# Kernel tuning notes

Measured on AMD Instinct MI355X. Metric: run time of the kernel, lower is better.

## Reference

```python
import jax, jax.numpy as jnp
import numpy as np

HEADS = 16
PHI = (1.0 + np.sqrt(5.0)) / 2.0


def setup_inputs() -> dict:
    key = jax.random.key(0)
    k1, k2, k3, k4 = jax.random.split(key, 4)
    B, L, D = 2, 2048, 1024
    x = jax.random.normal(k1, (B, L, D), dtype=jnp.float32)
    # nn.Linear(dim, 3*dim, bias=False): store as [D, 3D] for x @ W
    w_qkv = jax.random.normal(k2, (D, 3 * D), dtype=jnp.float32) * (D ** -0.5)
    w_proj = jax.random.normal(k3, (D, D), dtype=jnp.float32) * (D ** -0.5)
    b_proj = jax.random.normal(k4, (D,), dtype=jnp.float32) * 0.01
    return {"x": x, "w_qkv": w_qkv, "w_proj": w_proj, "b_proj": b_proj}


def phi_bias(L):
    # pos[i] = (i * phi) mod 1 ; bias = log(exp(-|pos_i - pos_j|) + 1e-8)
    pos = (jnp.arange(L, dtype=jnp.float32) * PHI) % 1.0
    dist = jnp.abs(pos[:, None] - pos[None, :])  # [L, L]
    return jnp.log(jnp.exp(-dist) + 1e-8)


def reference(x, w_qkv, w_proj, b_proj):
    B, L, D = x.shape
    H = HEADS
    Dh = D // H
    scale = Dh ** -0.5
    qkv = (x @ w_qkv).reshape(B, L, 3, H, Dh)
    q = jnp.transpose(qkv[:, :, 0], (0, 2, 1, 3))  # [B, H, L, Dh]
    k = jnp.transpose(qkv[:, :, 1], (0, 2, 1, 3))
    v = jnp.transpose(qkv[:, :, 2], (0, 2, 1, 3))
    attn = jnp.einsum("bhid,bhjd->bhij", q, k) * scale  # [B, H, L, L]
    attn = attn + phi_bias(L)[None, None]  # additive phi-distance bias
    attn = jax.nn.softmax(attn, axis=-1)
    out = jnp.einsum("bhij,bhjd->bhid", attn, v)  # [B, H, L, Dh]
    out = jnp.transpose(out, (0, 2, 1, 3)).reshape(B, L, D)
    return out @ w_proj + b_proj
```

## Files before the change

### kernel.cpp

```cpp
#include <hip/hip_runtime.h>
#include <math.h>


typedef _Float16 f16;
typedef _Float16 f16x4 __attribute__((ext_vector_type(4)));
typedef _Float16 f16x8 __attribute__((ext_vector_type(8)));
typedef float f32x4 __attribute__((ext_vector_type(4)));

#define MFMA32(a, b, c) __builtin_amdgcn_mfma_f32_16x16x32_f16(a, b, c, 0, 0, 0)

static constexpr int Bsz = 2, Lseq = 2048, Dm = 1024, H = 16, Dh = 64;
static constexpr int Mtot = Bsz * Lseq;
static constexpr int NQKV = 3 * Dm;
static constexpr float PHI_F = 1.61803398874989484820f;
static constexpr float LOG2E = 1.44269504088896f;
static constexpr float QS = 0.125f * LOG2E;
static constexpr float CSTEP = 0.55417527999932633f;

__device__ __forceinline__ void pk2(float a, float b, f16* d) {
  auto v = __builtin_amdgcn_cvt_pkrtz(a, b);
  d[0] = (f16)v[0];
  d[1] = (f16)v[1];
}

__device__ __forceinline__ void load16_to_lds(const f16* g, f16* l) {
  __builtin_amdgcn_global_load_lds(
      (const __attribute__((address_space(1))) unsigned int*)g,
      (__attribute__((address_space(3))) unsigned int*)l, 16, 0, 0);
}

__global__ __launch_bounds__(256) void prep_kernel(
    const float* __restrict__ x, const float* __restrict__ wqkv,
    const float* __restrict__ wproj, f16* __restrict__ xb,
    f16* __restrict__ wqkvT, f16* __restrict__ wpT) {
  __shared__ float tile[32][33];
  int bid = blockIdx.x, tid = threadIdx.x;
  if (bid < 4096) {
    int i = bid * 1024 + tid * 4;
    float4 v = *reinterpret_cast<const float4*>(x + i);
    f16 t[4] = {(f16)v.x, (f16)v.y, (f16)v.z, (f16)v.w};
    *reinterpret_cast<uint2*>(xb + i) = *reinterpret_cast<uint2*>(t);
    return;
  }
  const float* in;
  f16* out;
  int K, N, n0, k0;
  if (bid < 4096 + 3072) {
    int b2 = bid - 4096;
    in = wqkv; out = wqkvT; K = Dm; N = NQKV;
    n0 = (b2 % 96) * 32; k0 = (b2 / 96) * 32;
  } else {
    int b2 = bid - 7168;
    in = wproj; out = wpT; K = Dm; N = Dm;
    n0 = (b2 & 31) * 32; k0 = (b2 >> 5) * 32;
  }
  int tx = tid & 31, ty = tid >> 5;
#pragma unroll
  for (int r = 0; r < 32; r += 8)
    tile[ty + r][tx] = in[(size_t)(k0 + ty + r) * N + n0 + tx];
  __syncthreads();
#pragma unroll
  for (int r = 0; r < 32; r += 8)
    out[(size_t)(n0 + ty + r) * K + k0 + tx] = (f16)tile[tx][ty + r];
}

template <int MODE>
__global__ __launch_bounds__(256) void gemm_f16(
    const f16* __restrict__ A, const f16* __restrict__ Bt,
    int M, int N, int K,
    f16* __restrict__ qb, f16* __restrict__ kb, f16* __restrict__ vb,
    float* __restrict__ out, const float* __restrict__ bias) {
  constexpr int BM = (MODE == 0) ? 128 : 64;
  constexpr int MI = BM / 32;
  constexpr int AI = BM / 32;
  __shared__ f16 As[BM * 64];
  __shared__ f16 Bs[128 * 64];

  int tid = threadIdx.x;
  int wave = tid >> 6, lane = tid & 63;
  int quad = lane >> 4, l16 = lane & 15;
  int wm = (wave >> 1) * (MI * 16), wn = (wave & 1) * 64;

  int lid = blockIdx.x;
  int xcd = lid & 7, t = lid >> 3;
  int m0, n0;
  if (MODE == 0) {
    int mg = xcd >> 1, ng = xcd & 1;
    m0 = (mg * 8 + t / 12) * 128;
    n0 = (ng * 12 + t % 12) * 128;
  } else {
    m0 = (xcd * 8 + (t >> 3)) * 64;
    n0 = (t & 7) * 128;
  }

  const int gu = (lane & 7) ^ (lane >> 3);
  const f16* gA[AI];
  f16* lA[AI];
#pragma unroll
  for (int i = 0; i < AI; i++) {
    int it = wave * AI + i;
    gA[i] = A + (size_t)(m0 + it * 8 + (lane >> 3)) * K + gu * 8;
    lA[i] = As + it * 512;
  }
  const f16* gB[4];
  f16* lB[4];
#pragma unroll
  for (int i = 0; i < 4; i++) {
    int it = wave * 4 + i;
    gB[i] = Bt + (size_t)(n0 + it * 8 + (lane >> 3)) * K + gu * 8;
    lB[i] = Bs + it * 512;
  }

  f32x4 acc[MI][4] = {};

  for (int k0 = 0; k0 < K; k0 += 64) {
#pragma unroll
    for (int i = 0; i < AI; i++) load16_to_lds(gA[i] + k0, lA[i]);
#pragma unroll
    for (int i = 0; i < 4; i++) load16_to_lds(gB[i] + k0, lB[i]);
    __syncthreads();
#pragma unroll
    for (int s = 0; s < 2; s++) {
      f16x8 a[MI], b[4];
#pragma unroll
      for (int i = 0; i < MI; i++) {
        int row = wm + i * 16 + l16;
        a[i] = *reinterpret_cast<const f16x8*>(
            As + row * 64 + (((s * 4 + quad) ^ (l16 & 7)) * 8));
      }
#pragma unroll
      for (int j = 0; j < 4; j++) {
        int row = wn + j * 16 + l16;
        b[j] = *reinterpret_cast<const f16x8*>(
            Bs + row * 64 + (((s * 4 + quad) ^ (l16 & 7)) * 8));
      }
#pragma unroll
      for (int i = 0; i < MI; i++)
#pragma unroll
        for (int j = 0; j < 4; j++)
          acc[i][j] = MFMA32(a[i], b[j], acc[i][j]);
    }
    __syncthreads();
  }

  if (MODE == 1) {
#pragma unroll
    for (int i = 0; i < MI; i++)
#pragma unroll
      for (int j = 0; j < 4; j++) {
        int n = n0 + wn + j * 16 + l16;
#pragma unroll
        for (int r = 0; r < 4; r++) {
          int m = m0 + wm + i * 16 + quad * 4 + r;
          out[(size_t)m * N + n] = acc[i][j][r] + bias[n];
        }
      }
    return;
  }
  int ty = n0 >> 10;
  if (ty < 2) {
    f16* dst = (ty == 0) ? qb : kb;
    float sc = (ty == 0) ? QS : 1.0f;
#pragma unroll
    for (int i = 0; i < MI; i++)
#pragma unroll
      for (int j = 0; j < 4; j++) {
        int n = n0 + wn + j * 16 + l16;
        int h = (n & 1023) >> 6, dh = n & 63;
#pragma unroll
        for (int r = 0; r < 4; r++) {
          int m = m0 + wm + i * 16 + quad * 4 + r;
          int b = m >> 11, l = m & 2047;
          dst[(((size_t)(b * H + h)) * Lseq + l) * Dh + dh] =
              (f16)(acc[i][j][r] * sc);
        }
      }
  } else {
#pragma unroll
    for (int i = 0; i < MI; i++) {
      int mb = m0 + wm + i * 16 + quad * 4;
      int b = mb >> 11, l = mb & 2047;
      int L0 = l & ~63, lg = l & 63;
      int c = ((lg >> 5) << 2) | ((lg >> 2) & 3);
      int e0 = ((lg >> 4) & 1) * 4;
      int off = L0 + c * 8 + e0;
#pragma unroll
      for (int j = 0; j < 4; j++) {
        int n = n0 + wn + j * 16 + l16;
        int h = (n & 1023) >> 6, dh = n & 63;
        f16x4 v;
        pk2(acc[i][j][0], acc[i][j][1], (f16*)&v);
        pk2(acc[i][j][2], acc[i][j][3], ((f16*)&v) + 2);
        *reinterpret_cast<uint2*>(
            vb + ((size_t)(b * H + h) * Dh + dh) * Lseq + off) =
            *reinterpret_cast<uint2*>(&v);
      }
    }
  }
}

__global__ __launch_bounds__(256, 4) void attn_kernel(
    const f16* __restrict__ qb,
    const f16* __restrict__ kb,
    const f16* __restrict__ vb,
    f16* __restrict__ ctx) {
  __shared__ __align__(16) unsigned char smem[32768];
  f16* Ks0 = (f16*)smem;
  f16* Ks1 = (f16*)(smem + 8192);
  f16* Vs0 = (f16*)(smem + 16384);
  f16* Vs1 = (f16*)(smem + 24576);

  int bh = blockIdx.y;
  int q0 = blockIdx.x * 64;
  int tid = threadIdx.x, wave = tid >> 6, lane = tid & 63;
  int quad = lane >> 4, l16 = lane & 15;
  int jhalf = wave >> 1, qhalf = wave & 1;

  f16x8 qfrag[2][2];
  float pq[2];
#pragma unroll
  for (int set = 0; set < 2; set++) {
    int q = q0 + qhalf * 32 + set * 16 + l16;
    const f16* Qrow = qb + ((size_t)bh * Lseq + q) * Dh;
    qfrag[set][0] = *reinterpret_cast<const f16x8*>(Qrow + quad * 8);
    qfrag[set][1] = *reinterpret_cast<const f16x8*>(Qrow + 32 + quad * 8);
    pq[set] = fmodf((float)q * PHI_F, 1.0f);
  }

  float pk[2][4];
#pragma unroll
  for (int jb = 0; jb < 2; jb++)
#pragma unroll
    for (int r = 0; r < 4; r++) {
      int j = jhalf * 32 + jb * 16 + quad * 4 + r;
      pk[jb][r] = fmodf((float)j * PHI_F, 1.0f);
    }

  const f16* Kbh = kb + (size_t)bh * Lseq * Dh;
  const f16* Vbh = vb + (size_t)bh * Dh * Lseq;
  const int gu = (lane & 7) ^ (lane >> 3);
  const f16* gK[2];
  const f16* gV[2];
  f16* lK[2];
  f16* lV[2];
#pragma unroll
  for (int i = 0; i < 2; i++) {
    int g8 = (wave * 2 + i) * 8 + (lane >> 3);
    gK[i] = Kbh + (size_t)g8 * Dh + gu * 8;
    gV[i] = Vbh + (size_t)g8 * Lseq + gu * 8;
    lK[i] = Ks0 + (wave * 2 + i) * 512;
    lV[i] = Vs0 + (wave * 2 + i) * 512;
  }

  const f16 one = (f16)1.0f;
  const f16x8 ones8 = {one, one, one, one, one, one, one, one};

  f32x4 acc_o[2][4] = {};
  f32x4 acc_l[2] = {};

  auto phase = [&](const f16* Ksp, const f16* Vsp) {
    f32x4 accs[2][2] = {};
#pragma unroll
    for (int s = 0; s < 2; s++)
#pragma unroll
      for (int jb = 0; jb < 2; jb++) {
        f16x8 kf = *reinterpret_cast<const f16x8*>(
            Ksp + (jhalf * 32 + jb * 16 + l16) * 64 +
            (((s * 4 + quad) ^ (l16 & 7)) * 8));
        accs[0][jb] = MFMA32(kf, qfrag[0][s], accs[0][jb]);
        accs[1][jb] = MFMA32(kf, qfrag[1][s], accs[1][jb]);
      }
    f16x8 pf8[2];
#pragma unroll
    for (int set = 0; set < 2; set++) {
#pragma unroll
      for (int jb = 0; jb < 2; jb++) {
        float p[4];
#pragma unroll
        for (int r = 0; r < 4; r++) {
          float d = pq[set] - pk[jb][r];
          float arg = fmaf(-LOG2E, fabsf(d), accs[set][jb][r]);
          p[r] = __builtin_amdgcn_exp2f(arg);
        }
        pk2(p[0], p[1], ((f16*)&pf8[set]) + jb * 4);
        pk2(p[2], p[3], ((f16*)&pf8[set]) + jb * 4 + 2);
      }
      acc_l[set] = MFMA32(ones8, pf8[set], acc_l[set]);
    }
#pragma unroll
    for (int jb = 0; jb < 2; jb++)
#pragma unroll
      for (int r = 0; r < 4; r++)
        pk[jb][r] = __builtin_amdgcn_fractf(pk[jb][r] + CSTEP);
#pragma unroll
    for (int dblk = 0; dblk < 4; dblk++) {
      int row = dblk * 16 + l16;
      f16x8 va = *reinterpret_cast<const f16x8*>(
          Vsp + row * 64 + (((jhalf * 4 + quad) ^ (l16 & 7)) * 8));
      acc_o[0][dblk] = MFMA32(va, pf8[0], acc_o[0][dblk]);
      acc_o[1][dblk] = MFMA32(va, pf8[1], acc_o[1][dblk]);
    }
  };

  for (int j0 = 0; j0 < Lseq; j0 += 128) {
    __syncthreads();
#pragma unroll
    for (int i = 0; i < 2; i++) {
      load16_to_lds(gK[i] + (size_t)j0 * Dh, lK[i]);
      load16_to_lds(gK[i] + (size_t)(j0 + 64) * Dh, lK[i] + 4096);
      load16_to_lds(gV[i] + j0, lV[i]);
      load16_to_lds(gV[i] + j0 + 64, lV[i] + 4096);
    }
    __syncthreads();
    phase(Ks0, Vs0);
    phase(Ks1, Vs1);
  }

  __syncthreads();
  float* Oex = (float*)smem;
  float* Lex = (float*)(smem + 16384);
  if (jhalf == 1) {
#pragma unroll
    for (int set = 0; set < 2; set++) {
#pragma unroll
      for (int dblk = 0; dblk < 4; dblk++)
#pragma unroll
        for (int r = 0; r < 4; r++)
          Oex[(((qhalf * 2 + set) * 4 + dblk) * 16 + quad * 4 + r) * 16 + l16] =
              acc_o[set][dblk][r];
      if (quad == 0) Lex[(qhalf * 2 + set) * 16 + l16] = acc_l[set][0];
    }
  }
  __syncthreads();
  if (jhalf == 0) {
    int b = bh >> 4, h = bh & 15;
#pragma unroll
    for (int set = 0; set < 2; set++) {
      float ltot = acc_l[set][0] + Lex[(qhalf * 2 + set) * 16 + l16];
      float inv = 1.0f / ltot;
      int q = q0 + qhalf * 32 + set * 16 + l16;
      f16* crow = ctx + (size_t)(b * Lseq + q) * Dm + h * 64;
#pragma unroll
      for (int dblk = 0; dblk < 4; dblk++) {
        f16x4 o;
#pragma unroll
        for (int r = 0; r < 4; r++) {
          float full = acc_o[set][dblk][r] +
              Oex[(((qhalf * 2 + set) * 4 + dblk) * 16 + quad * 4 + r) * 16 + l16];
          o[r] = (f16)(full * inv);
        }
        *reinterpret_cast<uint2*>(crow + dblk * 16 + quad * 4) =
            *reinterpret_cast<uint2*>(&o);
      }
    }
  }
}

extern "C" void kernel_launch(void* const* d_in, const int* in_sizes, int n_in,
                              void* d_out, int out_size, void* d_ws, size_t ws_size,
                              hipStream_t stream) {
  const float* x      = (const float*)d_in[0];
  const float* w_qkv  = (const float*)d_in[1];
  const float* w_proj = (const float*)d_in[2];
  const float* b_proj = (const float*)d_in[3];
  float* out = (float*)d_out;

  f16* xb    = (f16*)d_ws;
  f16* wqkvT = xb + (size_t)Mtot * Dm;
  f16* wpT   = wqkvT + (size_t)NQKV * Dm;
  f16* qb    = wpT + (size_t)Dm * Dm;
  f16* kb    = qb + (size_t)Bsz * H * Lseq * Dh;
  f16* vb    = kb + (size_t)Bsz * H * Lseq * Dh;
  f16* ctx   = vb + (size_t)Bsz * H * Lseq * Dh;

  prep_kernel<<<8192, 256, 0, stream>>>(x, w_qkv, w_proj, xb, wqkvT, wpT);

  gemm_f16<0><<<768, 256, 0, stream>>>(
      xb, wqkvT, Mtot, NQKV, Dm, qb, kb, vb, nullptr, nullptr);

  attn_kernel<<<dim3(Lseq / 64, Bsz * H), 256, 0, stream>>>(qb, kb, vb, ctx);

  gemm_f16<1><<<512, 256, 0, stream>>>(
      ctx, wpT, Mtot, Dm, Dm, nullptr, nullptr, nullptr, out, b_proj);
}
```

Baseline: 194.4 us.

## Restructure attention to load K/V directly to registers with XCD-aware grid mapping

Drops the LDS staging of K/V tiles and the block-wide barriers. Each wave now reads K and V fragments straight from global memory into registers, double-buffered in software, and handles 64 queries over the full key range, so the cross-wave reduction of partial outputs is no longer needed. The grid shrinks to 256 blocks of 256 queries, and the block index is swizzled so that blocks sharing a batch-head land on the same XCD for L2 reuse. In exchange, each wave issues its own global loads, register pressure rises (launch bound 1), and only 256 workgroups run with lower occupancy.

```diff
diff --git a/kernel.cpp b/kernel.cpp
--- a/kernel.cpp
+++ b/kernel.cpp
@@ -15,7 +15,7 @@
 static constexpr float PHI_F = 1.61803398874989484820f;
 static constexpr float LOG2E = 1.44269504088896f;
 static constexpr float QS = 0.125f * LOG2E;
-static constexpr float CSTEP = 0.55417527999932633f;
+static constexpr float CSTEP32 = 0.77708763999663514f;
 
 __device__ __forceinline__ void pk2(float a, float b, f16* d) {
   auto v = __builtin_amdgcn_cvt_pkrtz(a, b);
@@ -199,28 +199,27 @@
   }
 }
 
-__global__ __launch_bounds__(256, 4) void attn_kernel(
+__global__ __launch_bounds__(256, 1) void attn_kernel(
     const f16* __restrict__ qb,
     const f16* __restrict__ kb,
     const f16* __restrict__ vb,
     f16* __restrict__ ctx) {
-  __shared__ __align__(16) unsigned char smem[32768];
-  f16* Ks0 = (f16*)smem;
-  f16* Ks1 = (f16*)(smem + 8192);
-  f16* Vs0 = (f16*)(smem + 16384);
-  f16* Vs1 = (f16*)(smem + 24576);
-
-  int bh = blockIdx.y;
-  int q0 = blockIdx.x * 64;
+  int bid = blockIdx.x;
+  int xcd = bid & 7, rr = bid >> 3;
+  int qblk = rr & 7, bgrp = rr >> 3;
+  int bh = bgrp * 8 + xcd;
   int tid = threadIdx.x, wave = tid >> 6, lane = tid & 63;
   int quad = lane >> 4, l16 = lane & 15;
-  int jhalf = wave >> 1, qhalf = wave & 1;
-
-  f16x8 qfrag[2][2];
-  float pq[2];
-#pragma unroll
-  for (int set = 0; set < 2; set++) {
-    int q = q0 + qhalf * 32 + set * 16 + l16;
+  int qw = qblk * 256 + wave * 64;
+
+  const f16* Kbh = kb + (size_t)bh * Lseq * Dh;
+  const f16* Vbh = vb + (size_t)bh * Dh * Lseq;
+
+  f16x8 qfrag[4][2];
+  float pq[4];
+#pragma unroll
+  for (int set = 0; set < 4; set++) {
+    int q = qw + set * 16 + l16;
     const f16* Qrow = qb + ((size_t)bh * Lseq + q) * Dh;
     qfrag[set][0] = *reinterpret_cast<const f16x8*>(Qrow + quad * 8);
     qfrag[set][1] = *reinterpret_cast<const f16x8*>(Qrow + 32 + quad * 8);
@@ -231,48 +230,61 @@
 #pragma unroll
   for (int jb = 0; jb < 2; jb++)
 #pragma unroll
-    for (int r = 0; r < 4; r++) {
-      int j = jhalf * 32 + jb * 16 + quad * 4 + r;
-      pk[jb][r] = fmodf((float)j * PHI_F, 1.0f);
-    }
-
-  const f16* Kbh = kb + (size_t)bh * Lseq * Dh;
-  const f16* Vbh = vb + (size_t)bh * Dh * Lseq;
-  const int gu = (lane & 7) ^ (lane >> 3);
-  const f16* gK[2];
-  const f16* gV[2];
-  f16* lK[2];
-  f16* lV[2];
-#pragma unroll
-  for (int i = 0; i < 2; i++) {
-    int g8 = (wave * 2 + i) * 8 + (lane >> 3);
-    gK[i] = Kbh + (size_t)g8 * Dh + gu * 8;
-    gV[i] = Vbh + (size_t)g8 * Lseq + gu * 8;
-    lK[i] = Ks0 + (wave * 2 + i) * 512;
-    lV[i] = Vs0 + (wave * 2 + i) * 512;
-  }
+    for (int r = 0; r < 4; r++)
+      pk[jb][r] = fmodf((float)(jb * 16 + quad * 4 + r) * PHI_F, 1.0f);
+
+  const f16* pK[2][2];
+#pragma unroll
+  for (int jb = 0; jb < 2; jb++)
+#pragma unroll
+    for (int s = 0; s < 2; s++)
+      pK[jb][s] = Kbh + (size_t)(jb * 16 + l16) * Dh + s * 32 + quad * 8;
+  const f16* pV[4];
+#pragma unroll
+  for (int d = 0; d < 4; d++)
+    pV[d] = Vbh + (size_t)(d * 16 + l16) * Lseq + quad * 8;
 
   const f16 one = (f16)1.0f;
   const f16x8 ones8 = {one, one, one, one, one, one, one, one};
 
-  f32x4 acc_o[2][4] = {};
-  f32x4 acc_l[2] = {};
-
-  auto phase = [&](const f16* Ksp, const f16* Vsp) {
-    f32x4 accs[2][2] = {};
+  f32x4 acc_o[4][4] = {};
+  f32x4 acc_l[4] = {};
+
+  f16x8 ka[2][2], vfa[4], kc[2][2], vfc[4];
+
+  auto loadA = [&](int p) {
+#pragma unroll
+    for (int jb = 0; jb < 2; jb++)
+#pragma unroll
+      for (int s = 0; s < 2; s++)
+        ka[jb][s] = *reinterpret_cast<const f16x8*>(pK[jb][s] + p * 2048);
+#pragma unroll
+    for (int d = 0; d < 4; d++)
+      vfa[d] = *reinterpret_cast<const f16x8*>(pV[d] + p * 32);
+  };
+  auto loadC = [&](int p) {
+#pragma unroll
+    for (int jb = 0; jb < 2; jb++)
+#pragma unroll
+      for (int s = 0; s < 2; s++)
+        kc[jb][s] = *reinterpret_cast<const f16x8*>(pK[jb][s] + p * 2048);
+#pragma unroll
+    for (int d = 0; d < 4; d++)
+      vfc[d] = *reinterpret_cast<const f16x8*>(pV[d] + p * 32);
+  };
+
+  auto compute = [&](f16x8 (&kf)[2][2], f16x8 (&vf)[4]) {
+    f32x4 accs[4][2] = {};
 #pragma unroll
     for (int s = 0; s < 2; s++)
 #pragma unroll
-      for (int jb = 0; jb < 2; jb++) {
-        f16x8 kf = *reinterpret_cast<const f16x8*>(
-            Ksp + (jhalf * 32 + jb * 16 + l16) * 64 +
-            (((s * 4 + quad) ^ (l16 & 7)) * 8));
-        accs[0][jb] = MFMA32(kf, qfrag[0][s], accs[0][jb]);
-        accs[1][jb] = MFMA32(kf, qfrag[1][s], accs[1][jb]);
-      }
-    f16x8 pf8[2];
-#pragma unroll
-    for (int set = 0; set < 2; set++) {
+      for (int jb = 0; jb < 2; jb++)
+#pragma unroll
+        for (int set = 0; set < 4; set++)
+          accs[set][jb] = MFMA32(kf[jb][s], qfrag[set][s], accs[set][jb]);
+    f16x8 pf8[4];
+#pragma unroll
+    for (int set = 0; set < 4; set++) {
 #pragma unroll
       for (int jb = 0; jb < 2; jb++) {
         float p[4];
@@ -291,67 +303,35 @@
     for (int jb = 0; jb < 2; jb++)
 #pragma unroll
       for (int r = 0; r < 4; r++)
-        pk[jb][r] = __builtin_amdgcn_fractf(pk[jb][r] + CSTEP);
+        pk[jb][r] = __builtin_amdgcn_fractf(pk[jb][r] + CSTEP32);
+#pragma unroll
+    for (int dblk = 0; dblk < 4; dblk++)
+#pragma unroll
+      for (int set = 0; set < 4; set++)
+        acc_o[set][dblk] = MFMA32(vf[dblk], pf8[set], acc_o[set][dblk]);
+  };
+
+  loadA(0);
+  for (int p = 0; p < 64; p += 2) {
+    loadC(p + 1);
+    compute(ka, vfa);
+    if (p + 2 < 64) loadA(p + 2);
+    compute(kc, vfc);
+  }
+
+  int b = bh >> 4, h = bh & 15;
+#pragma unroll
+  for (int set = 0; set < 4; set++) {
+    float inv = 1.0f / acc_l[set][0];
+    int q = qw + set * 16 + l16;
+    f16* crow = ctx + (size_t)(b * Lseq + q) * Dm + h * 64;
 #pragma unroll
     for (int dblk = 0; dblk < 4; dblk++) {
-      int row = dblk * 16 + l16;
-      f16x8 va = *reinterpret_cast<const f16x8*>(
-          Vsp + row * 64 + (((jhalf * 4 + quad) ^ (l16 & 7)) * 8));
-      acc_o[0][dblk] = MFMA32(va, pf8[0], acc_o[0][dblk]);
-      acc_o[1][dblk] = MFMA32(va, pf8[1], acc_o[1][dblk]);
-    }
-  };
-
-  for (int j0 = 0; j0 < Lseq; j0 += 128) {
-    __syncthreads();
-#pragma unroll
-    for (int i = 0; i < 2; i++) {
-      load16_to_lds(gK[i] + (size_t)j0 * Dh, lK[i]);
-      load16_to_lds(gK[i] + (size_t)(j0 + 64) * Dh, lK[i] + 4096);
-      load16_to_lds(gV[i] + j0, lV[i]);
-      load16_to_lds(gV[i] + j0 + 64, lV[i] + 4096);
-    }
-    __syncthreads();
-    phase(Ks0, Vs0);
-    phase(Ks1, Vs1);
-  }
-
-  __syncthreads();
-  float* Oex = (float*)smem;
-  float* Lex = (float*)(smem + 16384);
-  if (jhalf == 1) {
-#pragma unroll
-    for (int set = 0; set < 2; set++) {
-#pragma unroll
-      for (int dblk = 0; dblk < 4; dblk++)
-#pragma unroll
-        for (int r = 0; r < 4; r++)
-          Oex[(((qhalf * 2 + set) * 4 + dblk) * 16 + quad * 4 + r) * 16 + l16] =
-              acc_o[set][dblk][r];
-      if (quad == 0) Lex[(qhalf * 2 + set) * 16 + l16] = acc_l[set][0];
-    }
-  }
-  __syncthreads();
-  if (jhalf == 0) {
-    int b = bh >> 4, h = bh & 15;
-#pragma unroll
-    for (int set = 0; set < 2; set++) {
-      float ltot = acc_l[set][0] + Lex[(qhalf * 2 + set) * 16 + l16];
-      float inv = 1.0f / ltot;
-      int q = q0 + qhalf * 32 + set * 16 + l16;
-      f16* crow = ctx + (size_t)(b * Lseq + q) * Dm + h * 64;
-#pragma unroll
-      for (int dblk = 0; dblk < 4; dblk++) {
-        f16x4 o;
-#pragma unroll
-        for (int r = 0; r < 4; r++) {
-          float full = acc_o[set][dblk][r] +
-              Oex[(((qhalf * 2 + set) * 4 + dblk) * 16 + quad * 4 + r) * 16 + l16];
-          o[r] = (f16)(full * inv);
-        }
-        *reinterpret_cast<uint2*>(crow + dblk * 16 + quad * 4) =
-            *reinterpret_cast<uint2*>(&o);
-      }
+      f16x4 o;
+      pk2(acc_o[set][dblk][0] * inv, acc_o[set][dblk][1] * inv, (f16*)&o);
+      pk2(acc_o[set][dblk][2] * inv, acc_o[set][dblk][3] * inv, ((f16*)&o) + 2);
+      *reinterpret_cast<uint2*>(crow + dblk * 16 + quad * 4) =
+          *reinterpret_cast<uint2*>(&o);
     }
   }
 }
@@ -378,7 +358,7 @@
   gemm_f16<0><<<768, 256, 0, stream>>>(
       xb, wqkvT, Mtot, NQKV, Dm, qb, kb, vb, nullptr, nullptr);
 
-  attn_kernel<<<dim3(Lseq / 64, Bsz * H), 256, 0, stream>>>(qb, kb, vb, ctx);
+  attn_kernel<<<256, 256, 0, stream>>>(qb, kb, vb, ctx);
 
   gemm_f16<1><<<512, 256, 0, stream>>>(
       ctx, wpT, Mtot, Dm, Dm, nullptr, nullptr, nullptr, out, b_proj);
```

Result: slower. 201.9 us (+3.9%).
